# Kernel optimization log

Hardware: AMD Instinct MI355X
Metric: run time of the kernel (lower is better)

Reference implementation:

```python
import jax, jax.numpy as jnp
import numpy as np
import math

FACTOR = 5

def setup_inputs() -> dict:
    key = jax.random.key(0)
    k1, k2, k3, k4 = jax.random.split(key, 4)
    B, L, H, D = 2, 4096, 8, 64
    sample_k = min(FACTOR * int(np.ceil(np.log(L))), L)  # 45
    return {
        "queries": jax.random.normal(k1, (B, L, H, D), dtype=jnp.float32),
        "keys": jax.random.normal(k2, (B, L, H, D), dtype=jnp.float32),
        "values": jax.random.normal(k3, (B, L, H, D), dtype=jnp.float32),
        "attn_mask": jnp.zeros((1,), dtype=bool),  # unused (mask_flag=False)
        "index_sample": jax.random.randint(k4, (L, sample_k), 0, L, dtype=jnp.int64),
    }

def reference(queries, keys, values, attn_mask, index_sample):
    B, L_Q, H, D = queries.shape
    L_K = keys.shape[1]
    # [B,L,H,D] -> [B,H,L,D]
    q = jnp.transpose(queries, (0, 2, 1, 3))
    k = jnp.transpose(keys, (0, 2, 1, 3))
    v = jnp.transpose(values, (0, 2, 1, 3))

    n_top = min(FACTOR * int(np.ceil(np.log(L_Q))), L_Q)  # u

    # --- _prob_QK ---
    # K_sample[b,h,l,s,e] = k[b,h,index_sample[l,s],e]
    K_sample = k[:, :, index_sample, :]                      # [B,H,L_Q,S,E]
    Q_K_sample = jnp.einsum('bhle,bhlse->bhls', q, K_sample)  # [B,H,L_Q,S]
    # sparsity measure: max - mean(over full L_K as in torch code)
    M = Q_K_sample.max(axis=-1) - Q_K_sample.sum(axis=-1) / L_K  # [B,H,L_Q]
    M_top = jax.lax.top_k(M, n_top)[1]                        # [B,H,u] indices

    Q_reduce = jnp.take_along_axis(q, M_top[..., None], axis=2)  # [B,H,u,E]
    scores_top = jnp.einsum('bhue,bhke->bhuk', Q_reduce, k)      # [B,H,u,L_K]

    scale = 1.0 / math.sqrt(D)
    attn = jax.nn.softmax(scale * scores_top, axis=-1)           # [B,H,u,L_K]
    context_in_q = jnp.einsum('bhuk,bhkd->bhud', attn, v)        # [B,H,u,D]

    # scatter selected contexts into zero-initialized tensor
    b_idx = jnp.arange(B)[:, None, None]
    h_idx = jnp.arange(H)[None, :, None]
    context = jnp.zeros((B, H, L_Q, D), dtype=queries.dtype)
    context = context.at[b_idx, h_idx, M_top].set(context_in_q)

    return jnp.transpose(context, (0, 2, 1, 3))  # [B,L_Q,H,D]
```

## Files before the change

### kernel.cpp

```cpp
#include <hip/hip_runtime.h>
#include <math.h>

#define B_ 2
#define L_ 4096
#define H_ 8
#define D_ 64
#define S_ 45
#define NTOP_ 45
#define SCALE 0.125f
#define TKEYS 64
#define NSPLIT 64

template<int CTRL>
__device__ __forceinline__ float dpp_permf(float x) {
    return __int_as_float(__builtin_amdgcn_update_dpp(
        0, __float_as_int(x), CTRL, 0xF, 0xF, true));
}

__global__ __launch_bounds__(256) void compute_M_kernel(
    const float* __restrict__ q, const float* __restrict__ k,
    const int* __restrict__ samp, float* __restrict__ M) {
    __shared__ int sIdx[8 * 48];
    int tid = threadIdx.x;
    int g   = blockIdx.x;
    int xcd = g & 7;
    int chunk = g >> 3;
    int b  = xcd >> 2;
    int h0 = (xcd & 3) * 2;
    int l0 = chunk * 8;

    for (int i = tid; i < 8 * S_; i += 256) {
        int qq = i / S_, ss = i - qq * S_;
        sIdx[qq * 48 + ss] = samp[(long)(l0 + qq) * S_ + ss];
    }
    if (tid < 24) sIdx[(tid / 3) * 48 + S_ + (tid % 3)] = 0;
    __syncthreads();

    int lane = tid & 63, wave = tid >> 6;
    int c  = lane & 31;
    int q8 = wave * 2 + (lane >> 5);
    int l  = l0 + q8;

    float4 q4 = ((const float4*)(q + (((long)(b * L_ + l)) * H_ + h0) * D_))[c];
    const float4* kb4 = (const float4*)(k + ((long)b * L_ * H_ + h0) * (long)D_);
    const int* myIdx = sIdx + q8 * 48;

    float4 f0 = kb4[(long)myIdx[0] * 128 + c];
    float4 f1 = kb4[(long)myIdx[1] * 128 + c];
    float4 f2 = kb4[(long)myIdx[2] * 128 + c];

    float vmax = -INFINITY, vsum = 0.f;
    #pragma unroll 3
    for (int s = 0; s < S_; ++s) {
        float4 nf = kb4[(long)myIdx[s + 3] * 128 + c];
        float p = q4.x * f0.x + q4.y * f0.y + q4.z * f0.z + q4.w * f0.w;
        p += dpp_permf<0xB1>(p);
        p += dpp_permf<0x4E>(p);
        p += __shfl_xor(p, 4, 64);
        p += __shfl_xor(p, 8, 64);
        vmax = fmaxf(vmax, p);
        vsum += p;
        f0 = f1; f1 = f2; f2 = nf;
    }
    if ((lane & 15) == 0) {
        int h = h0 + ((lane >> 4) & 1);
        M[(long)(b * 8 + h) * L_ + l] = vmax - vsum * (1.0f / (float)L_);
    }
}

__global__ __launch_bounds__(256) void topk_kernel(
    const float* __restrict__ M, int* __restrict__ topIdx) {
    __shared__ unsigned int hist[256];
    __shared__ unsigned int suf[257];
    __shared__ unsigned int wsum[4];
    __shared__ int sBin, sRemain, sCnt, sTieCnt;
    __shared__ int tie[64];

    int bh = blockIdx.x, tid = threadIdx.x;
    int lane = tid & 63, wave = tid >> 6;
    const float* row = M + (long)bh * L_;

    unsigned int key[16];
    #pragma unroll
    for (int j = 0; j < 16; ++j) {
        unsigned int bts = __float_as_uint(row[tid + 256 * j]);
        key[j] = bts ^ ((unsigned int)((int)bts >> 31) | 0x80000000u);
    }

    unsigned int prefix = 0, pmask = 0;
    int remain = NTOP_;
    #pragma unroll 1
    for (int pass = 3; pass >= 0; --pass) {
        int shift = pass * 8;
        hist[tid] = 0;
        __syncthreads();
        #pragma unroll
        for (int j = 0; j < 16; ++j) {
            if ((key[j] & pmask) == prefix)
                atomicAdd(&hist[(key[j] >> shift) & 255u], 1u);
        }
        __syncthreads();
        unsigned int s = hist[tid];
        #pragma unroll
        for (int off = 1; off < 64; off <<= 1) {
            unsigned int o = __shfl_down(s, off, 64);
            if (lane + off < 64) s += o;
        }
        if (lane == 0) wsum[wave] = s;
        __syncthreads();
        unsigned int add = 0;
        for (int w = wave + 1; w < 4; ++w) add += wsum[w];
        s += add;
        suf[tid] = s;
        if (tid == 0) suf[256] = 0;
        __syncthreads();
        if (suf[tid] >= (unsigned int)remain && suf[tid + 1] < (unsigned int)remain) {
            sBin = tid;
            sRemain = remain - (int)suf[tid + 1];
        }
        __syncthreads();
        prefix |= ((unsigned int)sBin) << shift;
        pmask  |= 0xFFu << shift;
        remain  = sRemain;
        __syncthreads();
    }

    if (tid == 0) { sCnt = 0; sTieCnt = 0; }
    __syncthreads();
    int* outRow = topIdx + bh * NTOP_;
    #pragma unroll
    for (int j = 0; j < 16; ++j) {
        int idx = tid + 256 * j;
        if (key[j] > prefix) {
            int pos = atomicAdd(&sCnt, 1);
            outRow[pos] = idx;
        } else if (key[j] == prefix) {
            int tp = atomicAdd(&sTieCnt, 1);
            if (tp < 64) tie[tp] = idx;
        }
    }
    __syncthreads();
    if (tid == 0) {
        int base = sCnt;
        int tc = sTieCnt < 64 ? sTieCnt : 64;
        for (int t = 0; t < remain; ++t) {
            int mi = 0x7fffffff, mj = 0;
            for (int j2 = 0; j2 < tc; ++j2)
                if (tie[j2] < mi) { mi = tie[j2]; mj = j2; }
            outRow[base + t] = mi;
            tie[mj] = 0x7fffffff;
        }
    }
}

#define STRIDE 68
__global__ __launch_bounds__(256, 2) void attn_strip_kernel(
    const float* __restrict__ q, const float* __restrict__ k,
    const float* __restrict__ v, const int* __restrict__ topIdx,
    float* __restrict__ pOut, float* __restrict__ plPart, int nsplit) {
    __shared__ float sQ[48 * STRIDE];
    __shared__ float sK[TKEYS * STRIDE];
    __shared__ float sV[TKEYS * STRIDE];
    __shared__ float sP[48 * STRIDE];

    int g = blockIdx.x;
    int xcd = g & 7;
    int s0 = g >> 3;
    int grp = s0 / nsplit;
    int bh = xcd + 8 * grp;
    int split = s0 - grp * nsplit;
    int b = bh >> 3, h = bh & 7;
    int tid = threadIdx.x;
    int key0 = split * TKEYS;

    #pragma unroll
    for (int j = 0; j < 3; ++j) {
        int i = tid + 256 * j;
        int u = i >> 4, d4 = i & 15;
        float4 val = make_float4(0.f, 0.f, 0.f, 0.f);
        if (u < NTOP_) {
            int lq = topIdx[bh * NTOP_ + u];
            val = *(const float4*)(q + (((long)(b * L_ + lq)) * H_ + h) * D_ + 4 * d4);
        }
        *(float4*)(sQ + u * STRIDE + 4 * d4) = val;
    }
    #pragma unroll
    for (int j = 0; j < 4; ++j) {
        int i = tid + 256 * j;
        int r = i >> 4, d4 = i & 15;
        long off = (((long)(b * L_ + key0 + r)) * H_ + h) * D_ + 4 * d4;
        *(float4*)(sK + r * STRIDE + 4 * d4) = *(const float4*)(k + off);
        *(float4*)(sV + r * STRIDE + 4 * d4) = *(const float4*)(v + off);
    }
    __syncthreads();

    int tx = tid & 15, ty = tid >> 4;
    float acc[3][4];
    #pragma unroll
    for (int i = 0; i < 3; ++i)
        #pragma unroll
        for (int j = 0; j < 4; ++j) acc[i][j] = 0.f;

    #pragma unroll 4
    for (int d4 = 0; d4 < 16; ++d4) {
        float4 qv[3];
        #pragma unroll
        for (int i = 0; i < 3; ++i)
            qv[i] = *(const float4*)(sQ + (3 * ty + i) * STRIDE + 4 * d4);
        #pragma unroll
        for (int j = 0; j < 4; ++j) {
            float4 kv = *(const float4*)(sK + (tx + 16 * j) * STRIDE + 4 * d4);
            #pragma unroll
            for (int i = 0; i < 3; ++i)
                acc[i][j] += qv[i].x * kv.x + qv[i].y * kv.y + qv[i].z * kv.z + qv[i].w * kv.w;
        }
    }
    #pragma unroll
    for (int i = 0; i < 3; ++i) {
        #pragma unroll
        for (int j = 0; j < 4; ++j)
            sP[(3 * ty + i) * STRIDE + tx + 16 * j] = __expf(acc[i][j] * SCALE);
    }
    __syncthreads();

    int dx = tid & 15, uy = tid >> 4;
    float o[3][4];
    float ls[3];
    #pragma unroll
    for (int i = 0; i < 3; ++i) {
        ls[i] = 0.f;
        #pragma unroll
        for (int c = 0; c < 4; ++c) o[i][c] = 0.f;
    }
    #pragma unroll 4
    for (int k4 = 0; k4 < 16; ++k4) {
        float pa[3][4];
        #pragma unroll
        for (int i = 0; i < 3; ++i)
            *(float4*)pa[i] = *(const float4*)(sP + (3 * uy + i) * STRIDE + 4 * k4);
        #pragma unroll
        for (int c = 0; c < 4; ++c) {
            float4 vr = *(const float4*)(sV + (4 * k4 + c) * STRIDE + 4 * dx);
            #pragma unroll
            for (int i = 0; i < 3; ++i) {
                o[i][0] += pa[i][c] * vr.x;
                o[i][1] += pa[i][c] * vr.y;
                o[i][2] += pa[i][c] * vr.z;
                o[i][3] += pa[i][c] * vr.w;
                ls[i]   += pa[i][c];
            }
        }
    }
    #pragma unroll
    for (int i = 0; i < 3; ++i) {
        int u = 3 * uy + i;
        if (u < NTOP_) {
            long base = ((long)(split * 16 + bh) * NTOP_ + u) * D_;
            *(float4*)(pOut + base + 4 * dx) = make_float4(o[i][0], o[i][1], o[i][2], o[i][3]);
            if (dx == 0) plPart[(long)(split * 16 + bh) * NTOP_ + u] = ls[i];
        }
    }
}

__global__ __launch_bounds__(256) void zero_reduce_scatter_kernel(
    const int* __restrict__ topIdx, const float* __restrict__ pOut,
    const float* __restrict__ plPart, float* __restrict__ out, int nsplit) {
    __shared__ int sTop[8 * NTOP_];
    __shared__ int sel[256];
    __shared__ int selCnt;
    int g = blockIdx.x;
    int b = g >> 7;
    int l0 = (g & 127) * 32;
    int tid = threadIdx.x;
    if (tid == 0) selCnt = 0;
    for (int i = tid; i < 8 * NTOP_; i += 256) sTop[i] = topIdx[b * 8 * NTOP_ + i];
    __syncthreads();

    float4* obase = (float4*)(out + ((long)(b * L_ + l0)) * H_ * D_);
    float4 z = make_float4(0.f, 0.f, 0.f, 0.f);
    #pragma unroll
    for (int j = 0; j < 16; ++j) obase[tid + 256 * j] = z;

    {
        int l = l0 + (tid >> 3), h = tid & 7;
        const int* rowp = sTop + h * NTOP_;
        int u = -1;
        #pragma unroll
        for (int t = 0; t < NTOP_; ++t)
            if (rowp[t] == l) u = t;
        if (u >= 0) { int p = atomicAdd(&selCnt, 1); sel[p] = (tid << 8) | u; }
    }
    __syncthreads();

    int lane = tid & 63, wave = tid >> 6;
    int n = selCnt;
    for (int w = wave; w < n; w += 4) {
        int e = sel[w];
        int t = e >> 8, u = e & 255;
        int l = l0 + (t >> 3), h = t & 7, bh = b * 8 + h;
        float lv = (lane < nsplit) ? plPart[((long)lane * 16 + bh) * NTOP_ + u] : 0.f;
        #pragma unroll
        for (int o = 32; o > 0; o >>= 1) lv += __shfl_xor(lv, o, 64);
        float accv = 0.f;
        const float* pb = pOut + ((long)bh * NTOP_ + u) * D_ + lane;
        #pragma unroll 8
        for (int s = 0; s < nsplit; ++s) accv += pb[(long)s * 16 * NTOP_ * D_];
        out[(((long)(b * L_ + l)) * H_ + h) * D_ + lane] = accv / lv;
    }
}

extern "C" void kernel_launch(void* const* d_in, const int* in_sizes, int n_in,
                              void* d_out, int out_size, void* d_ws, size_t ws_size,
                              hipStream_t stream) {
    const float* q = (const float*)d_in[0];
    const float* k = (const float*)d_in[1];
    const float* v = (const float*)d_in[2];
    const int* samp = (const int*)d_in[4];
    float* out = (float*)d_out;

    char* ws = (char*)d_ws;
    const size_t mBytes   = (size_t)B_ * H_ * L_ * sizeof(float);
    const size_t topBytes = (size_t)B_ * H_ * NTOP_ * sizeof(int);
    const size_t plBytes  = (size_t)NSPLIT * 16 * NTOP_ * sizeof(float);
    float* M      = (float*)ws;
    int*   topIdx = (int*)(ws + mBytes);
    float* plPart = (float*)(ws + mBytes + topBytes);
    float* pOut   = (float*)(ws + mBytes + topBytes + plBytes);

    int nsplit = NSPLIT;
    while (nsplit > 1) {
        size_t need = mBytes + topBytes + plBytes +
                      (size_t)nsplit * 16 * NTOP_ * D_ * sizeof(float);
        if (need <= ws_size) break;
        nsplit >>= 1;
    }

    compute_M_kernel<<<4096, 256, 0, stream>>>(q, k, samp, M);

    topk_kernel<<<B_ * H_, 256, 0, stream>>>(M, topIdx);

    attn_strip_kernel<<<nsplit * B_ * H_, 256, 0, stream>>>(
        q, k, v, topIdx, pOut, plPart, nsplit);

    zero_reduce_scatter_kernel<<<B_ * (L_ / 32), 256, 0, stream>>>(
        topIdx, pOut, plPart, out, nsplit);
}
```

Measured before the change: 163.5 us.

## Replace single-block radix top-k with two-stage chunked rank-based top-k

```diff
diff --git a/kernel.cpp b/kernel.cpp
--- a/kernel.cpp
+++ b/kernel.cpp
@@ -68,89 +68,50 @@
     }
 }
 
-__global__ __launch_bounds__(256) void topk_kernel(
-    const float* __restrict__ M, int* __restrict__ topIdx) {
-    __shared__ unsigned int hist[256];
-    __shared__ unsigned int suf[257];
-    __shared__ unsigned int wsum[4];
-    __shared__ int sBin, sRemain, sCnt, sTieCnt;
-    __shared__ int tie[64];
-
+__global__ __launch_bounds__(256) void chunk_topk_kernel(
+    const float* __restrict__ M, unsigned long long* __restrict__ cand) {
+    __shared__ unsigned long long sKey[256];
+    int g = blockIdx.x;
+    int bh = g >> 4, chunk = g & 15;
+    int tid = threadIdx.x;
+    int l = chunk * 256 + tid;
+    unsigned int bts = __float_as_uint(M[(long)bh * L_ + l]);
+    unsigned int mapped = bts ^ ((unsigned int)((int)bts >> 31) | 0x80000000u);
+    unsigned long long key =
+        ((unsigned long long)mapped << 32) | (unsigned long long)(0xFFFFFFFFu - (unsigned int)l);
+    sKey[tid] = key;
+    __syncthreads();
+    int rank = 0;
+    #pragma unroll 16
+    for (int j = 0; j < 256; ++j)
+        rank += (sKey[j] > key) ? 1 : 0;
+    if (rank < NTOP_)
+        cand[((long)bh * 16 + chunk) * NTOP_ + rank] = key;
+}
+
+__global__ __launch_bounds__(256) void merge_topk_kernel(
+    const unsigned long long* __restrict__ cand, int* __restrict__ topIdx) {
+    __shared__ unsigned long long sKey[16 * NTOP_];
     int bh = blockIdx.x, tid = threadIdx.x;
-    int lane = tid & 63, wave = tid >> 6;
-    const float* row = M + (long)bh * L_;
-
-    unsigned int key[16];
-    #pragma unroll
-    for (int j = 0; j < 16; ++j) {
-        unsigned int bts = __float_as_uint(row[tid + 256 * j]);
-        key[j] = bts ^ ((unsigned int)((int)bts >> 31) | 0x80000000u);
-    }
-
-    unsigned int prefix = 0, pmask = 0;
-    int remain = NTOP_;
-    #pragma unroll 1
-    for (int pass = 3; pass >= 0; --pass) {
-        int shift = pass * 8;
-        hist[tid] = 0;
-        __syncthreads();
-        #pragma unroll
-        for (int j = 0; j < 16; ++j) {
-            if ((key[j] & pmask) == prefix)
-                atomicAdd(&hist[(key[j] >> shift) & 255u], 1u);
-        }
-        __syncthreads();
-        unsigned int s = hist[tid];
-        #pragma unroll
-        for (int off = 1; off < 64; off <<= 1) {
-            unsigned int o = __shfl_down(s, off, 64);
-            if (lane + off < 64) s += o;
-        }
-        if (lane == 0) wsum[wave] = s;
-        __syncthreads();
-        unsigned int add = 0;
-        for (int w = wave + 1; w < 4; ++w) add += wsum[w];
-        s += add;
-        suf[tid] = s;
-        if (tid == 0) suf[256] = 0;
-        __syncthreads();
-        if (suf[tid] >= (unsigned int)remain && suf[tid + 1] < (unsigned int)remain) {
-            sBin = tid;
-            sRemain = remain - (int)suf[tid + 1];
-        }
-        __syncthreads();
-        prefix |= ((unsigned int)sBin) << shift;
-        pmask  |= 0xFFu << shift;
-        remain  = sRemain;
-        __syncthreads();
-    }
-
-    if (tid == 0) { sCnt = 0; sTieCnt = 0; }
-    __syncthreads();
+    for (int i = tid; i < 16 * NTOP_; i += 256)
+        sKey[i] = cand[(long)bh * 16 * NTOP_ + i];
+    __syncthreads();
+    unsigned long long k0 = sKey[tid];
+    unsigned long long k1 = sKey[tid + 256];
+    bool has2 = (tid + 512) < 16 * NTOP_;
+    unsigned long long k2 = has2 ? sKey[tid + 512] : 0ull;
+    int r0 = 0, r1 = 0, r2 = 0;
+    #pragma unroll 8
+    for (int j = 0; j < 16 * NTOP_; ++j) {
+        unsigned long long kj = sKey[j];
+        r0 += (kj > k0) ? 1 : 0;
+        r1 += (kj > k1) ? 1 : 0;
+        r2 += (kj > k2) ? 1 : 0;
+    }
     int* outRow = topIdx + bh * NTOP_;
-    #pragma unroll
-    for (int j = 0; j < 16; ++j) {
-        int idx = tid + 256 * j;
-        if (key[j] > prefix) {
-            int pos = atomicAdd(&sCnt, 1);
-            outRow[pos] = idx;
-        } else if (key[j] == prefix) {
-            int tp = atomicAdd(&sTieCnt, 1);
-            if (tp < 64) tie[tp] = idx;
-        }
-    }
-    __syncthreads();
-    if (tid == 0) {
-        int base = sCnt;
-        int tc = sTieCnt < 64 ? sTieCnt : 64;
-        for (int t = 0; t < remain; ++t) {
-            int mi = 0x7fffffff, mj = 0;
-            for (int j2 = 0; j2 < tc; ++j2)
-                if (tie[j2] < mi) { mi = tie[j2]; mj = j2; }
-            outRow[base + t] = mi;
-            tie[mj] = 0x7fffffff;
-        }
-    }
+    if (r0 < NTOP_) outRow[r0] = (int)(0xFFFFFFFFu - (unsigned int)(k0 & 0xFFFFFFFFull));
+    if (r1 < NTOP_) outRow[r1] = (int)(0xFFFFFFFFu - (unsigned int)(k1 & 0xFFFFFFFFull));
+    if (has2 && r2 < NTOP_) outRow[r2] = (int)(0xFFFFFFFFu - (unsigned int)(k2 & 0xFFFFFFFFull));
 }
 
 #define STRIDE 68
@@ -319,25 +280,31 @@
     float* out = (float*)d_out;
 
     char* ws = (char*)d_ws;
-    const size_t mBytes   = (size_t)B_ * H_ * L_ * sizeof(float);
-    const size_t topBytes = (size_t)B_ * H_ * NTOP_ * sizeof(int);
-    const size_t plBytes  = (size_t)NSPLIT * 16 * NTOP_ * sizeof(float);
+    const size_t mBytes    = (size_t)B_ * H_ * L_ * sizeof(float);
+    const size_t topBytes  = (size_t)B_ * H_ * NTOP_ * sizeof(int);
+    const size_t plBytes   = (size_t)NSPLIT * 16 * NTOP_ * sizeof(float);
+    const size_t poutBytes = (size_t)NSPLIT * 16 * NTOP_ * D_ * sizeof(float);
     float* M      = (float*)ws;
     int*   topIdx = (int*)(ws + mBytes);
     float* plPart = (float*)(ws + mBytes + topBytes);
     float* pOut   = (float*)(ws + mBytes + topBytes + plBytes);
+    unsigned long long* cand =
+        (unsigned long long*)(ws + mBytes + topBytes + plBytes + poutBytes);
 
     int nsplit = NSPLIT;
     while (nsplit > 1) {
         size_t need = mBytes + topBytes + plBytes +
-                      (size_t)nsplit * 16 * NTOP_ * D_ * sizeof(float);
+                      (size_t)nsplit * 16 * NTOP_ * D_ * sizeof(float) +
+                      (size_t)B_ * H_ * 16 * NTOP_ * sizeof(unsigned long long);
         if (need <= ws_size) break;
         nsplit >>= 1;
     }
 
     compute_M_kernel<<<4096, 256, 0, stream>>>(q, k, samp, M);
 
-    topk_kernel<<<B_ * H_, 256, 0, stream>>>(M, topIdx);
+    chunk_topk_kernel<<<B_ * H_ * 16, 256, 0, stream>>>(M, cand);
+
+    merge_topk_kernel<<<B_ * H_, 256, 0, stream>>>(cand, topIdx);
 
     attn_strip_kernel<<<nsplit * B_ * H_, 256, 0, stream>>>(
         q, k, v, topIdx, pOut, plPart, nsplit);
```

Measured after the change: 172.6 us. +5.6%, slower.

## Fuse output zeroing into attention kernel and reduce per selected query

Applied to the files above, without the earlier changes.

```diff
diff --git a/kernel.cpp b/kernel.cpp
--- a/kernel.cpp
+++ b/kernel.cpp
@@ -157,7 +157,8 @@
 __global__ __launch_bounds__(256, 2) void attn_strip_kernel(
     const float* __restrict__ q, const float* __restrict__ k,
     const float* __restrict__ v, const int* __restrict__ topIdx,
-    float* __restrict__ pOut, float* __restrict__ plPart, int nsplit) {
+    float* __restrict__ pOut, float* __restrict__ plPart,
+    float* __restrict__ out, int nsplit) {
     __shared__ float sQ[48 * STRIDE];
     __shared__ float sK[TKEYS * STRIDE];
     __shared__ float sV[TKEYS * STRIDE];
@@ -191,6 +192,14 @@
         long off = (((long)(b * L_ + key0 + r)) * H_ + h) * D_ + 4 * d4;
         *(float4*)(sK + r * STRIDE + 4 * d4) = *(const float4*)(k + off);
         *(float4*)(sV + r * STRIDE + 4 * d4) = *(const float4*)(v + off);
+    }
+
+    {
+        long total4 = (long)B_ * L_ * H_ * D_ / 4;
+        long per = total4 / ((long)nsplit * 16);
+        float4* ob = (float4*)out + (long)g * per;
+        float4 z = make_float4(0.f, 0.f, 0.f, 0.f);
+        for (long j = tid; j < per; j += 256) ob[j] = z;
     }
     __syncthreads();
 
@@ -262,50 +271,28 @@
     }
 }
 
-__global__ __launch_bounds__(256) void zero_reduce_scatter_kernel(
+__global__ __launch_bounds__(256) void reduce_norm_kernel(
     const int* __restrict__ topIdx, const float* __restrict__ pOut,
     const float* __restrict__ plPart, float* __restrict__ out, int nsplit) {
-    __shared__ int sTop[8 * NTOP_];
-    __shared__ int sel[256];
-    __shared__ int selCnt;
-    int g = blockIdx.x;
-    int b = g >> 7;
-    int l0 = (g & 127) * 32;
+    __shared__ float part[4][64];
+    __shared__ float lpart[4];
+    int u = blockIdx.x, bh = blockIdx.y;
+    int b = bh >> 3, h = bh & 7;
     int tid = threadIdx.x;
-    if (tid == 0) selCnt = 0;
-    for (int i = tid; i < 8 * NTOP_; i += 256) sTop[i] = topIdx[b * 8 * NTOP_ + i];
-    __syncthreads();
-
-    float4* obase = (float4*)(out + ((long)(b * L_ + l0)) * H_ * D_);
-    float4 z = make_float4(0.f, 0.f, 0.f, 0.f);
-    #pragma unroll
-    for (int j = 0; j < 16; ++j) obase[tid + 256 * j] = z;
-
-    {
-        int l = l0 + (tid >> 3), h = tid & 7;
-        const int* rowp = sTop + h * NTOP_;
-        int u = -1;
-        #pragma unroll
-        for (int t = 0; t < NTOP_; ++t)
-            if (rowp[t] == l) u = t;
-        if (u >= 0) { int p = atomicAdd(&selCnt, 1); sel[p] = (tid << 8) | u; }
-    }
-    __syncthreads();
-
-    int lane = tid & 63, wave = tid >> 6;
-    int n = selCnt;
-    for (int w = wave; w < n; w += 4) {
-        int e = sel[w];
-        int t = e >> 8, u = e & 255;
-        int l = l0 + (t >> 3), h = t & 7, bh = b * 8 + h;
-        float lv = (lane < nsplit) ? plPart[((long)lane * 16 + bh) * NTOP_ + u] : 0.f;
-        #pragma unroll
-        for (int o = 32; o > 0; o >>= 1) lv += __shfl_xor(lv, o, 64);
-        float accv = 0.f;
-        const float* pb = pOut + ((long)bh * NTOP_ + u) * D_ + lane;
-        #pragma unroll 8
-        for (int s = 0; s < nsplit; ++s) accv += pb[(long)s * 16 * NTOP_ * D_];
-        out[(((long)(b * L_ + l)) * H_ + h) * D_ + lane] = accv / lv;
+    int d = tid & 63, sg = tid >> 6;
+    float acc = 0.f, lsum = 0.f;
+    for (int s = sg; s < nsplit; s += 4) {
+        acc  += pOut[((long)(s * 16 + bh) * NTOP_ + u) * D_ + d];
+        lsum += plPart[(long)(s * 16 + bh) * NTOP_ + u];
+    }
+    part[sg][d] = acc;
+    if (d == 0) lpart[sg] = lsum;
+    __syncthreads();
+    if (sg == 0) {
+        float a = part[0][d] + part[1][d] + part[2][d] + part[3][d];
+        float lt = lpart[0] + lpart[1] + lpart[2] + lpart[3];
+        int lq = topIdx[bh * NTOP_ + u];
+        out[(((long)(b * L_ + lq)) * H_ + h) * D_ + d] = a / lt;
     }
 }
 
@@ -340,8 +327,8 @@
     topk_kernel<<<B_ * H_, 256, 0, stream>>>(M, topIdx);
 
     attn_strip_kernel<<<nsplit * B_ * H_, 256, 0, stream>>>(
-        q, k, v, topIdx, pOut, plPart, nsplit);
-
-    zero_reduce_scatter_kernel<<<B_ * (L_ / 32), 256, 0, stream>>>(
-        topIdx, pOut, plPart, out, nsplit);
-}
+        q, k, v, topIdx, pOut, plPart, out, nsplit);
+
+    dim3 gn(NTOP_, B_ * H_);
+    reduce_norm_kernel<<<gn, 256, 0, stream>>>(topIdx, pOut, plPart, out, nsplit);
+}
```

After: 155.3 us. -5.0%, faster.
